# Kernel optimization log

Measured on AMD Instinct MI355X. Metric: run time of the kernel, lower is better.

Reference implementation:

```python
import jax, jax.numpy as jnp
import numpy as np
from itertools import combinations

S = 7                       # number of species (H,C,N,O,S,F,Cl)
RCR, RCA = 5.2, 3.5         # radial / angular cutoffs (Angstrom)
ETA_R, ETA_A, ZETA = 19.7, 12.5, 14.1
SHF_R = jnp.asarray(0.8 + 0.275 * np.arange(16), jnp.float32)        # 16 radial shifts
SHF_A = jnp.asarray(0.8 + 0.3375 * np.arange(8), jnp.float32)        # 8 angular radial shifts
SHF_Z = jnp.asarray((np.arange(4) + 0.5) * np.pi / 4, jnp.float32)   # 4 angle shifts
NPAIR = S * (S + 1) // 2    # 28 unordered species pairs
_t = np.zeros((S, S), np.int32); _c = 0
for _a in range(S):
    for _b in range(_a, S):
        _t[_a, _b] = _t[_b, _a] = _c; _c += 1
TRIU = jnp.asarray(_t)
AEV_DIM = S * 16 + NPAIR * 32   # 1008
M, H1, H2, H3 = 8, 256, 192, 160  # ensemble size and MLP widths


def _fc(d, rc):
    # torchani cutoff_cosine, masked for safety beyond rc
    return jnp.where(d < rc, 0.5 * jnp.cos(jnp.pi * d / rc) + 0.5, 0.0)


def compute_aev(sp, coords, atom_index12, triplet_index):
    # sp:[N] int, coords:[N,3], atom_index12:[2,P] half neighbor list,
    # triplet_index:[3,T] = (center, neighbor_j, neighbor_k)
    N = sp.shape[0]
    i, j = atom_index12[0], atom_index12[1]
    dvec = coords[j] - coords[i]
    dist = jnp.sqrt((dvec * dvec).sum(-1))
    fc = _fc(dist, RCR)
    rterm = 0.25 * jnp.exp(-ETA_R * (dist[:, None] - SHF_R) ** 2) * fc[:, None]  # [P,16]
    rad = jnp.zeros((N * S, 16), rterm.dtype)
    rad = rad.at[i * S + sp[j]].add(rterm).at[j * S + sp[i]].add(rterm)
    rad = rad.reshape(N, S * 16)

    c, a, b = triplet_index[0], triplet_index[1], triplet_index[2]
    v1 = coords[a] - coords[c]
    v2 = coords[b] - coords[c]
    d1 = jnp.sqrt((v1 * v1).sum(-1))
    d2 = jnp.sqrt((v2 * v2).sum(-1))
    cosang = 0.95 * (v1 * v2).sum(-1) / (d1 * d2)   # 0.95 numerical-safety factor as in torchani
    ang = jnp.arccos(cosang)
    fcj = _fc(d1, RCA) * _fc(d2, RCA)
    f1 = ((1.0 + jnp.cos(ang[:, None] - SHF_Z)) / 2.0) ** ZETA              # [T,4]
    f2 = jnp.exp(-ETA_A * ((d1 + d2)[:, None] / 2.0 - SHF_A) ** 2)          # [T,8]
    aterm = 2.0 * (f2[:, :, None] * f1[:, None, :]).reshape(-1, 32) * fcj[:, None]  # [T,32]
    pidx = TRIU[sp[a], sp[b]]
    angv = jnp.zeros((N * NPAIR, 32), aterm.dtype).at[c * NPAIR + pidx].add(aterm)
    return jnp.concatenate([rad, angv.reshape(N, NPAIR * 32)], axis=-1)     # [N,1008]


def _energy_and_force(species, coordinates, atom_index12, triplet_index, sgp,
                      W1, b1, W2, b2, W3, b3, W4, b4, sae):
    sp = species[0]
    sgpv = sgp[0]

    def total(coords):
        aev = compute_aev(sp, coords[0], atom_index12, triplet_index)       # [N,1008]
        h = jax.nn.celu(jnp.einsum('na,msab->msnb', aev, W1) + b1[:, :, None, :], alpha=0.1)
        h = jax.nn.celu(jnp.einsum('msnb,msbc->msnc', h, W2) + b2[:, :, None, :], alpha=0.1)
        h = jax.nn.celu(jnp.einsum('msnc,mscd->msnd', h, W3) + b3[:, :, None, :], alpha=0.1)
        e = jnp.einsum('msnd,msd->msn', h, W4) + b4[:, :, None]             # [M,S,N]
        onehot = (sgpv[None, :] == jnp.arange(S)[:, None]).astype(e.dtype)  # ghosts (-1) -> all-zero
        atomic = (e * onehot[None]).sum(1).mean(0)                           # [N] ensemble mean
        atomic = atomic + jnp.where(sgpv >= 0, sae[jnp.clip(sgpv, 0)], 0.0)  # energy shifter SAEs
        return atomic.sum()

    E = total(coordinates)
    force = -jax.grad(total)(coordinates)   # autograd force as in forward_total
    return E[None], force


def setup_inputs() -> dict:
    key = jax.random.key(0)
    n = 14; N = n ** 3   # 2744 atoms on a jittered cubic lattice (2.5 A spacing)
    ar = np.arange(n)
    gx, gy, gz = np.meshgrid(ar, ar, ar, indexing='ij')
    pos = np.stack([gx, gy, gz], -1).reshape(-1, 3)
    lid = lambda p: (p[:, 0] * n + p[:, 1]) * n + p[:, 2]
    # half neighbor list: all lattice offsets with |r| <= 5.2/2.5 lattice units
    half = [(1,0,0),(0,1,0),(0,0,1),(1,1,0),(1,-1,0),(1,0,1),(1,0,-1),(0,1,1),(0,1,-1),
            (1,1,1),(1,1,-1),(1,-1,1),(1,-1,-1),(2,0,0),(0,2,0),(0,0,2)]
    ei, ej = [], []
    for off in half:
        q = pos + np.array(off)
        m = ((q >= 0) & (q < n)).all(1)
        ei.append(lid(pos[m])); ej.append(lid(q[m]))
    atom_index12 = np.stack([np.concatenate(ei), np.concatenate(ej)]).astype(np.int32)
    # angular triplets: pairs of unit-offset neighbors (within Rca=3.5 A) per center
    unit = [(1,0,0),(-1,0,0),(0,1,0),(0,-1,0),(0,0,1),(0,0,-1)]
    nb = np.full((N, 6), -1, np.int64)
    for t, off in enumerate(unit):
        q = pos + np.array(off)
        m = ((q >= 0) & (q < n)).all(1)
        nb[lid(pos[m]), t] = lid(q[m])
    tc, tj, tk = [], [], []
    for a_, b_ in combinations(range(6), 2):
        m = (nb[:, a_] >= 0) & (nb[:, b_] >= 0)
        tc.append(np.nonzero(m)[0]); tj.append(nb[m, a_]); tk.append(nb[m, b_])
    triplet_index = np.stack([np.concatenate(tc), np.concatenate(tj), np.concatenate(tk)]).astype(np.int32)
    rng = np.random.default_rng(0)
    species = rng.integers(0, S, (1, N)).astype(np.int32)
    nghost = 250
    sgp = species.copy(); sgp[0, N - nghost:] = -1   # ghost atoms padded with -1
    coords = (pos.astype(np.float32) * 2.5 + 0.15 * rng.standard_normal((N, 3)).astype(np.float32))[None]
    ks = jax.random.split(key, 9)
    D = AEV_DIM
    W1 = jax.random.normal(ks[0], (M, S, D, H1), jnp.float32) * (D ** -0.5)
    b1 = 0.01 * jax.random.normal(ks[1], (M, S, H1), jnp.float32)
    W2 = jax.random.normal(ks[2], (M, S, H1, H2), jnp.float32) * (H1 ** -0.5)
    b2 = 0.01 * jax.random.normal(ks[3], (M, S, H2), jnp.float32)
    W3 = jax.random.normal(ks[4], (M, S, H2, H3), jnp.float32) * (H2 ** -0.5)
    b3 = 0.01 * jax.random.normal(ks[5], (M, S, H3), jnp.float32)
    W4 = jax.random.normal(ks[6], (M, S, H3), jnp.float32) * (H3 ** -0.5)
    b4 = 0.01 * jax.random.normal(ks[7], (M, S), jnp.float32)
    sae = jax.random.normal(ks[8], (S,), jnp.float32)
    return {
        'species': jnp.asarray(species), 'coordinates': jnp.asarray(coords),
        'atom_index12': jnp.asarray(atom_index12), 'triplet_index': jnp.asarray(triplet_index),
        'species_ghost_as_padding': jnp.asarray(sgp),
        'W1': W1, 'b1': b1, 'W2': W2, 'b2': b2, 'W3': W3, 'b3': b3, 'W4': W4, 'b4': b4, 'sae': sae,
    }


def reference(species, coordinates, atom_index12, triplet_index, species_ghost_as_padding,
              W1, b1, W2, b2, W3, b3, W4, b4, sae):
    return _energy_and_force(species, coordinates, atom_index12, triplet_index,
                             species_ghost_as_padding, W1, b1, W2, b2, W3, b3, W4, b4, sae)
```

## Files before the change

kernel.cpp:

```cpp
#include <hip/hip_runtime.h>
#include <math.h>

constexpr int SPEC = 7;
constexpr int DAEV = 1008;
constexpr int RADN = 112;
constexpr int H1W = 256, H2W = 192, H3W = 160;
constexpr int MENS = 8;
constexpr float ALPHA = 0.1f;
constexpr float RCR_ = 5.2f, RCA_ = 3.5f;
constexpr float ETAR = 19.7f, ETAA = 12.5f, ZETA_ = 14.1f;
constexpr float PIF = 3.14159265358979323846f;

enum { MODE_FWD = 0, MODE_BWD = 1, MODE_PLAIN = 2 };

typedef _Float16 f16x8 __attribute__((ext_vector_type(8)));
typedef float f32x4 __attribute__((ext_vector_type(4)));

__device__ __forceinline__ f32x4 mfma16(f16x8 a, f16x8 b, f32x4 c) {
    return __builtin_amdgcn_mfma_f32_16x16x32_f16(a, b, c, 0, 0, 0);
}

__device__ __forceinline__ void cvt8(float4 u0, float4 u1, f16x8& h, f16x8& l) {
    float x[8] = {u0.x, u0.y, u0.z, u0.w, u1.x, u1.y, u1.z, u1.w};
    #pragma unroll
    for (int e = 0; e < 8; ++e) {
        _Float16 hh = (_Float16)x[e];
        h[e] = hh;
        l[e] = (_Float16)(x[e] - (float)hh);
    }
}

__global__ __launch_bounds__(256) void build_lists_k(
    const int* __restrict__ sgp, int* __restrict__ counts,
    int* __restrict__ lists, int N)
{
    int n = blockIdx.x * blockDim.x + threadIdx.x;
    if (n >= N) return;
    int g = sgp[n];
    if (g >= 0) {
        int p = atomicAdd(&counts[g], 1);
        lists[g * N + p] = n;
    }
}

__global__ __launch_bounds__(256) void radial_fwd_k(
    const int* __restrict__ ai12, const int* __restrict__ spec,
    const float* __restrict__ coord, float* __restrict__ aev, int P)
{
    int p = blockIdx.x * blockDim.x + threadIdx.x;
    if (p >= P) return;
    int i = ai12[p], j = ai12[P + p];
    float dx = coord[3 * j + 0] - coord[3 * i + 0];
    float dy = coord[3 * j + 1] - coord[3 * i + 1];
    float dz = coord[3 * j + 2] - coord[3 * i + 2];
    float d = sqrtf(dx * dx + dy * dy + dz * dz);
    float fc = (d < RCR_) ? (0.5f * cosf(PIF * d / RCR_) + 0.5f) : 0.f;
    int spi = spec[i], spj = spec[j];
    float* bi = aev + (size_t)i * DAEV + spj * 16;
    float* bj = aev + (size_t)j * DAEV + spi * 16;
    #pragma unroll
    for (int k = 0; k < 16; ++k) {
        float sh = 0.8f + 0.275f * k;
        float t = d - sh;
        float v = 0.25f * expf(-ETAR * t * t) * fc;
        atomicAdd(bi + k, v);
        atomicAdd(bj + k, v);
    }
}

__global__ __launch_bounds__(256) void angular_fwd_k(
    const int* __restrict__ tri, const int* __restrict__ spec,
    const float* __restrict__ coord, float* __restrict__ aev, int T)
{
    int t = blockIdx.x * blockDim.x + threadIdx.x;
    if (t >= T) return;
    int c = tri[t], a = tri[T + t], b = tri[2 * T + t];
    float cx = coord[3 * c], cy = coord[3 * c + 1], cz = coord[3 * c + 2];
    float v1x = coord[3 * a] - cx, v1y = coord[3 * a + 1] - cy, v1z = coord[3 * a + 2] - cz;
    float v2x = coord[3 * b] - cx, v2y = coord[3 * b + 1] - cy, v2z = coord[3 * b + 2] - cz;
    float d1 = sqrtf(v1x * v1x + v1y * v1y + v1z * v1z);
    float d2 = sqrtf(v2x * v2x + v2y * v2y + v2z * v2z);
    float u = v1x * v2x + v1y * v2y + v1z * v2z;
    float ca = 0.95f * u / (d1 * d2);
    float sa = sqrtf(fmaxf(1.f - ca * ca, 0.f));
    float fc1 = (d1 < RCA_) ? (0.5f * cosf(PIF * d1 / RCA_) + 0.5f) : 0.f;
    float fc2 = (d2 < RCA_) ? (0.5f * cosf(PIF * d2 / RCA_) + 0.5f) : 0.f;
    float fcj = fc1 * fc2;
    float savg = 0.5f * (d1 + d2);
    int s1 = spec[a], s2 = spec[b];
    int lo = min(s1, s2), hi = max(s1, s2);
    int pidx = lo * SPEC - (lo * (lo - 1)) / 2 + (hi - lo);
    float* ob = aev + (size_t)c * DAEV + RADN + pidx * 32;
    const float CZ[4] = {0.92387953f, 0.38268343f, -0.38268343f, -0.92387953f};
    const float SZ[4] = {0.38268343f, 0.92387953f, 0.92387953f, 0.38268343f};
    float f1[4];
    #pragma unroll
    for (int zz = 0; zz < 4; ++zz) {
        float cd = ca * CZ[zz] + sa * SZ[zz];
        float base = fmaxf(0.5f * (1.f + cd), 0.f);
        f1[zz] = powf(base, ZETA_);
    }
    #pragma unroll
    for (int q = 0; q < 8; ++q) {
        float sh = 0.8f + 0.3375f * q;
        float tq = savg - sh;
        float f2 = expf(-ETAA * tq * tq);
        float b2 = 2.f * f2 * fcj;
        #pragma unroll
        for (int zz = 0; zz < 4; ++zz)
            atomicAdd(ob + q * 4 + zz, b2 * f1[zz]);
    }
}

template<bool DO_O, bool DO_T>
__global__ __launch_bounds__(256) void wconv_k(
    const float* __restrict__ W,
    _Float16* __restrict__ oH, _Float16* __restrict__ oL,
    _Float16* __restrict__ tH, _Float16* __restrict__ tL,
    int K, int C, int ldt)
{
    __shared__ _Float16 sh[64][65];
    __shared__ _Float16 sl[64][65];
    const int z = blockIdx.z;
    const int k0 = blockIdx.y * 64, c0 = blockIdx.x * 64;
    const float* Wz = W + (size_t)z * K * C;
    const int c = threadIdx.x & 63, qr = threadIdx.x >> 6;
    #pragma unroll
    for (int rr = 0; rr < 16; ++rr) {
        int r = qr * 16 + rr;
        int k = k0 + r, cc = c0 + c;
        float v = (k < K && cc < C) ? Wz[(size_t)k * C + cc] : 0.f;
        _Float16 h = (_Float16)v;
        _Float16 l = (_Float16)(v - (float)h);
        if (DO_O && k < K && cc < C) {
            oH[(size_t)z * K * C + (size_t)k * C + cc] = h;
            oL[(size_t)z * K * C + (size_t)k * C + cc] = l;
        }
        if (DO_T) { sh[r][c] = h; sl[r][c] = l; }
    }
    if (DO_T) {
        __syncthreads();
        #pragma unroll
        for (int rr = 0; rr < 16; ++rr) {
            int r = qr * 16 + rr;
            int crow = c0 + r, kcol = k0 + c;
            if (crow < C && kcol < ldt) {
                tH[(size_t)z * C * ldt + (size_t)crow * ldt + kcol] = sh[c][r];
                tL[(size_t)z * C * ldt + (size_t)crow * ldt + kcol] = sl[c][r];
            }
        }
    }
}

template<int MODE, int ASRC, int BSRC, bool MCONCAT, int SPLITK>
__global__ __launch_bounds__(256) void mgemm_k(
    const void* __restrict__ Ah_, const void* __restrict__ Al_,
    const void* __restrict__ Bh_, const void* __restrict__ Bl_,
    const float* __restrict__ bias, float* __restrict__ cF,
    _Float16* __restrict__ cH, _Float16* __restrict__ cL,
    const int* __restrict__ lists, const int* __restrict__ counts,
    int N, int K, int KA, int H, int lda, int ldb, int ldc,
    size_t aStrM, size_t bStrZ, size_t cStrM)
{
    __shared__ f16x8 AhS[4][64];
    __shared__ f16x8 AlS[4][64];
    __shared__ f16x8 BhS[4][128];
    __shared__ f16x8 BlS[4][128];
    __shared__ int atomsS[64];

    const int z = blockIdx.z;
    int m, sp_, chunk;
    if (MCONCAT) {
        sp_ = (SPLITK > 1) ? (z % SPEC) : z;
        chunk = (SPLITK > 1) ? (z / SPEC) : 0;
        m = 0;
    } else {
        m = z / SPEC; sp_ = z - m * SPEC; chunk = 0;
    }
    const int cnt = counts[sp_];
    const int row0 = blockIdx.y * 64;
    if (row0 >= cnt) return;
    const int col0 = blockIdx.x * 128;
    const int tid = threadIdx.x;
    const int w = tid >> 6, lane = tid & 63;

    const int rA = min(row0 + lane, cnt - 1);
    const int atomA = lists[sp_ * N + rA];
    if (tid < 64) atomsS[tid] = atomA;

    const int bc0 = min(col0 + lane, H - 1);
    const int bc1 = min(col0 + 64 + lane, H - 1);

    f16x8 rAh, rAl;
    float4 rAf0, rAf1;
    f16x8 rBh0, rBl0, rBh1, rBl1;
    float4 rBq[4];
    float rB0f[8], rB1f[8];

    auto LOAD = [&](int k0s) {
        int kk = k0s + w * 8;
        if constexpr (ASRC == 0) {
            const _Float16* ah = (const _Float16*)Ah_;
            const _Float16* al = (const _Float16*)Al_;
            size_t ao;
            if constexpr (MCONCAT) {
                int mm = kk >> 8, kr = kk & 255;
                ao = ((size_t)mm * N + atomA) * (size_t)lda + kr;
            } else {
                ao = (size_t)m * aStrM + (size_t)atomA * lda + kk;
            }
            rAh = *(const f16x8*)(ah + ao);
            rAl = *(const f16x8*)(al + ao);
        } else {
            const float* af = (const float*)Ah_;
            if (kk < KA) {
                const float* p = af + (size_t)atomA * lda + kk;
                rAf0 = *(const float4*)p;
                rAf1 = *(const float4*)(p + 4);
            } else {
                rAf0 = make_float4(0.f, 0.f, 0.f, 0.f);
                rAf1 = rAf0;
            }
        }
        if constexpr (BSRC == 0) {
            const _Float16* bh = (const _Float16*)Bh_;
            const _Float16* bl = (const _Float16*)Bl_;
            size_t b0 = (size_t)z * bStrZ + (size_t)bc0 * ldb + kk;
            size_t b1 = (size_t)z * bStrZ + (size_t)bc1 * ldb + kk;
            rBh0 = *(const f16x8*)(bh + b0);
            rBh1 = *(const f16x8*)(bh + b1);
            rBl0 = *(const f16x8*)(bl + b0);
            rBl1 = *(const f16x8*)(bl + b1);
        } else if constexpr (BSRC == 1) {
            const float* bf = (const float*)Bh_;
            int mm = kk >> 8, kr = kk & 255;
            size_t b0 = ((size_t)(mm * SPEC + sp_) * DAEV + bc0) * (size_t)ldb + kr;
            size_t b1 = ((size_t)(mm * SPEC + sp_) * DAEV + bc1) * (size_t)ldb + kr;
            rBq[0] = *(const float4*)(bf + b0);
            rBq[1] = *(const float4*)(bf + b0 + 4);
            rBq[2] = *(const float4*)(bf + b1);
            rBq[3] = *(const float4*)(bf + b1 + 4);
        } else {
            const float* bf = (const float*)Bh_ + (size_t)z * bStrZ;
            #pragma unroll
            for (int j = 0; j < 8; ++j) {
                int kg = kk + j;
                float v0 = 0.f, v1 = 0.f;
                if (kg < KA) {
                    v0 = bf[(size_t)kg * ldb + bc0];
                    v1 = bf[(size_t)kg * ldb + bc1];
                }
                rB0f[j] = v0;
                rB1f[j] = v1;
            }
        }
    };

    auto WRITE = [&]() {
        if constexpr (ASRC == 0) {
            AhS[w][lane] = rAh;
            AlS[w][lane] = rAl;
        } else {
            f16x8 h, l;
            cvt8(rAf0, rAf1, h, l);
            AhS[w][lane] = h;
            AlS[w][lane] = l;
        }
        if constexpr (BSRC == 0) {
            BhS[w][lane] = rBh0;
            BhS[w][64 + lane] = rBh1;
            BlS[w][lane] = rBl0;
            BlS[w][64 + lane] = rBl1;
        } else if constexpr (BSRC == 1) {
            f16x8 h, l;
            cvt8(rBq[0], rBq[1], h, l);
            BhS[w][lane] = h;
            BlS[w][lane] = l;
            cvt8(rBq[2], rBq[3], h, l);
            BhS[w][64 + lane] = h;
            BlS[w][64 + lane] = l;
        } else {
            f16x8 h0, l0, h1, l1;
            #pragma unroll
            for (int j = 0; j < 8; ++j) {
                _Float16 ha = (_Float16)rB0f[j];
                h0[j] = ha; l0[j] = (_Float16)(rB0f[j] - (float)ha);
                _Float16 hb = (_Float16)rB1f[j];
                h1[j] = hb; l1[j] = (_Float16)(rB1f[j] - (float)hb);
            }
            BhS[w][lane] = h0;
            BlS[w][lane] = l0;
            BhS[w][64 + lane] = h1;
            BlS[w][64 + lane] = l1;
        }
    };

    const int wr = w >> 1, wc = w & 1;
    const int fr = lane & 15, q = lane >> 4;

    f32x4 acc[2][4];
    #pragma unroll
    for (int mi = 0; mi < 2; ++mi)
        #pragma unroll
        for (int ni = 0; ni < 4; ++ni)
            acc[mi][ni] = (f32x4){0.f, 0.f, 0.f, 0.f};

    const int KC = (SPLITK > 1) ? (K / SPLITK) : K;
    const int kbeg = chunk * KC;
    const int nt = KC / 32;
    LOAD(kbeg);

    for (int t = 0; t < nt; ++t) {
        __syncthreads();
        WRITE();
        __syncthreads();
        if (t + 1 < nt) LOAD(kbeg + (t + 1) * 32);

        f16x8 fah[2], fal[2], fbh[4], fbl[4];
        #pragma unroll
        for (int mi = 0; mi < 2; ++mi) {
            int r = wr * 32 + mi * 16 + fr;
            fah[mi] = AhS[q][r];
            fal[mi] = AlS[q][r];
        }
        #pragma unroll
        for (int ni = 0; ni < 4; ++ni) {
            int c = wc * 64 + ni * 16 + fr;
            fbh[ni] = BhS[q][c];
            fbl[ni] = BlS[q][c];
        }
        #pragma unroll
        for (int mi = 0; mi < 2; ++mi)
            #pragma unroll
            for (int ni = 0; ni < 4; ++ni) {
                acc[mi][ni] = mfma16(fah[mi], fbl[ni], acc[mi][ni]);
                acc[mi][ni] = mfma16(fal[mi], fbh[ni], acc[mi][ni]);
                acc[mi][ni] = mfma16(fah[mi], fbh[ni], acc[mi][ni]);
            }
    }

    const float* brow = (MODE == MODE_FWD) ? (bias + (size_t)z * H) : nullptr;
    #pragma unroll
    for (int mi = 0; mi < 2; ++mi) {
        #pragma unroll
        for (int r = 0; r < 4; ++r) {
            int rl = wr * 32 + mi * 16 + q * 4 + r;
            if (row0 + rl >= cnt) continue;
            int atom = atomsS[rl];
            size_t rowoff = (size_t)m * cStrM + (size_t)atom * ldc;
            #pragma unroll
            for (int ni = 0; ni < 4; ++ni) {
                int col = col0 + wc * 64 + ni * 16 + fr;
                if (col >= H) continue;
                float v = acc[mi][ni][r];
                size_t idx = rowoff + col;
                if (MODE == MODE_FWD) {
                    v += brow[col];
                    v = (v > 0.f) ? v : ALPHA * expm1f(v * (1.f / ALPHA));
                    _Float16 hh = (_Float16)v;
                    cH[idx] = hh;
                    cL[idx] = (_Float16)(v - (float)hh);
                } else if (MODE == MODE_BWD) {
                    float hprev = (float)cH[idx] + (float)cL[idx];
                    float D = (hprev > 0.f) ? 1.f : (hprev * (1.f / ALPHA) + 1.f);
                    v *= D;
                    _Float16 hh = (_Float16)v;
                    cH[idx] = hh;
                    cL[idx] = (_Float16)(v - (float)hh);
                } else {
                    if (SPLITK > 1) atomicAdd(cF + idx, v);
                    else cF[idx] = v;
                }
            }
        }
    }
}

__global__ __launch_bounds__(256) void l4_k(
    _Float16* __restrict__ h3H, _Float16* __restrict__ h3L,
    const float* __restrict__ W4, const float* __restrict__ b4,
    const int* __restrict__ lists, const int* __restrict__ counts,
    float* __restrict__ Eout, int N)
{
    const int z = blockIdx.y;
    const int m = z / SPEC, s = z - m * SPEC;
    const int cnt = counts[s];
    const int sub = threadIdx.x >> 3;
    const int l8 = threadIdx.x & 7;
    const int row = blockIdx.x * 32 + sub;

    __shared__ float bsum;
    if (threadIdx.x == 0) bsum = 0.f;
    __syncthreads();

    if (row < cnt) {
        int atom = lists[s * N + row];
        size_t base = ((size_t)m * N + atom) * H3W;
        const float* w4 = W4 + (size_t)z * H3W;
        float sum = 0.f;
        for (int k = l8; k < H3W; k += 8) {
            float h = (float)h3H[base + k] + (float)h3L[base + k];
            float wv = w4[k];
            sum += h * wv;
            float D = (h > 0.f) ? 1.f : (h * 10.f + 1.f);
            float g = 0.125f * wv * D;
            _Float16 gh = (_Float16)g;
            h3H[base + k] = gh;
            h3L[base + k] = (_Float16)(g - (float)gh);
        }
        sum += __shfl_xor(sum, 1);
        sum += __shfl_xor(sum, 2);
        sum += __shfl_xor(sum, 4);
        if (l8 == 0) atomicAdd(&bsum, sum + b4[z]);
    }
    __syncthreads();
    if (threadIdx.x == 0) atomicAdd(Eout, 0.125f * bsum);
}

__global__ __launch_bounds__(256) void radial_bwd_k(
    const int* __restrict__ ai12, const int* __restrict__ spec,
    const float* __restrict__ coord, const float* __restrict__ daev,
    float* __restrict__ grad, int P)
{
    int p = blockIdx.x * blockDim.x + threadIdx.x;
    if (p >= P) return;
    int i = ai12[p], j = ai12[P + p];
    float dx = coord[3 * j + 0] - coord[3 * i + 0];
    float dy = coord[3 * j + 1] - coord[3 * i + 1];
    float dz = coord[3 * j + 2] - coord[3 * i + 2];
    float d = sqrtf(dx * dx + dy * dy + dz * dz);
    float fc, dfc;
    if (d < RCR_) {
        float ph = PIF * d / RCR_;
        fc = 0.5f * cosf(ph) + 0.5f;
        dfc = -0.5f * sinf(ph) * (PIF / RCR_);
    } else { fc = 0.f; dfc = 0.f; }
    int spi = spec[i], spj = spec[j];
    const float* gi = daev + (size_t)i * DAEV + spj * 16;
    const float* gj = daev + (size_t)j * DAEV + spi * 16;
    float gs = 0.f;
    #pragma unroll
    for (int k = 0; k < 16; ++k) {
        float sh = 0.8f + 0.275f * k;
        float t = d - sh;
        float ex = expf(-ETAR * t * t);
        float g = gi[k] + gj[k];
        gs += g * 0.25f * ex * (dfc - 2.f * ETAR * t * fc);
    }
    float invd = 1.f / d;
    float gx = gs * dx * invd, gy = gs * dy * invd, gz = gs * dz * invd;
    atomicAdd(&grad[3 * j + 0], gx);  atomicAdd(&grad[3 * j + 1], gy);  atomicAdd(&grad[3 * j + 2], gz);
    atomicAdd(&grad[3 * i + 0], -gx); atomicAdd(&grad[3 * i + 1], -gy); atomicAdd(&grad[3 * i + 2], -gz);
}

__global__ __launch_bounds__(256) void angular_bwd_k(
    const int* __restrict__ tri, const int* __restrict__ spec,
    const float* __restrict__ coord, const float* __restrict__ daev,
    float* __restrict__ grad, int T)
{
    int t = blockIdx.x * blockDim.x + threadIdx.x;
    if (t >= T) return;
    int c = tri[t], a = tri[T + t], b = tri[2 * T + t];
    float cx = coord[3 * c], cy = coord[3 * c + 1], cz = coord[3 * c + 2];
    float v1x = coord[3 * a] - cx, v1y = coord[3 * a + 1] - cy, v1z = coord[3 * a + 2] - cz;
    float v2x = coord[3 * b] - cx, v2y = coord[3 * b + 1] - cy, v2z = coord[3 * b + 2] - cz;
    float d1 = sqrtf(v1x * v1x + v1y * v1y + v1z * v1z);
    float d2 = sqrtf(v2x * v2x + v2y * v2y + v2z * v2z);
    float u = v1x * v2x + v1y * v2y + v1z * v2z;
    float inv12 = 1.f / (d1 * d2);
    float ca = 0.95f * u * inv12;
    float sa = sqrtf(fmaxf(1.f - ca * ca, 1e-12f));
    float fc1, dfc1, fc2, dfc2;
    if (d1 < RCA_) {
        float ph = PIF * d1 / RCA_;
        fc1 = 0.5f * cosf(ph) + 0.5f;
        dfc1 = -0.5f * sinf(ph) * (PIF / RCA_);
    } else { fc1 = 0.f; dfc1 = 0.f; }
    if (d2 < RCA_) {
        float ph = PIF * d2 / RCA_;
        fc2 = 0.5f * cosf(ph) + 0.5f;
        dfc2 = -0.5f * sinf(ph) * (PIF / RCA_);
    } else { fc2 = 0.f; dfc2 = 0.f; }
    float fcj = fc1 * fc2;
    float savg = 0.5f * (d1 + d2);
    int s1 = spec[a], s2 = spec[b];
    int lo = min(s1, s2), hi = max(s1, s2);
    int pidx = lo * SPEC - (lo * (lo - 1)) / 2 + (hi - lo);
    const float* gb = daev + (size_t)c * DAEV + RADN + pidx * 32;
    const float CZ[4] = {0.92387953f, 0.38268343f, -0.38268343f, -0.92387953f};
    const float SZ[4] = {0.38268343f, 0.92387953f, 0.92387953f, 0.38268343f};
    float f1[4], df1[4];
    #pragma unroll
    for (int zz = 0; zz < 4; ++zz) {
        float cd = ca * CZ[zz] + sa * SZ[zz];
        float sd = sa * CZ[zz] - ca * SZ[zz];
        float base = fmaxf(0.5f * (1.f + cd), 0.f);
        float pm1 = powf(base, ZETA_ - 1.f);
        f1[zz] = pm1 * base;
        df1[zz] = ZETA_ * pm1 * (-0.5f * sd);
    }
    float A_ = 0.f, B_ = 0.f, Cc = 0.f;
    #pragma unroll
    for (int q = 0; q < 8; ++q) {
        float sh = 0.8f + 0.3375f * q;
        float tq = savg - sh;
        float f2 = expf(-ETAA * tq * tq);
        float df2 = -ETAA * tq * f2;
        #pragma unroll
        for (int zz = 0; zz < 4; ++zz) {
            float G2 = 2.f * gb[q * 4 + zz];
            A_ += G2 * f2 * df1[zz];
            B_ += G2 * df2 * f1[zz];
            Cc += G2 * f2 * f1[zz];
        }
    }
    A_ *= fcj; B_ *= fcj;
    float C1 = Cc * dfc1 * fc2;
    float C2 = Cc * fc1 * dfc2;
    float cA = -A_ / sa;
    float k12 = cA * 0.95f * inv12;
    float coef1 = (cA * (-ca) / d1 + B_ + C1) / d1;
    float coef2 = (cA * (-ca) / d2 + B_ + C2) / d2;
    float g1x = coef1 * v1x + k12 * v2x;
    float g1y = coef1 * v1y + k12 * v2y;
    float g1z = coef1 * v1z + k12 * v2z;
    float g2x = coef2 * v2x + k12 * v1x;
    float g2y = coef2 * v2y + k12 * v1y;
    float g2z = coef2 * v2z + k12 * v1z;
    atomicAdd(&grad[3 * a + 0], g1x); atomicAdd(&grad[3 * a + 1], g1y); atomicAdd(&grad[3 * a + 2], g1z);
    atomicAdd(&grad[3 * b + 0], g2x); atomicAdd(&grad[3 * b + 1], g2y); atomicAdd(&grad[3 * b + 2], g2z);
    atomicAdd(&grad[3 * c + 0], -(g1x + g2x));
    atomicAdd(&grad[3 * c + 1], -(g1y + g2y));
    atomicAdd(&grad[3 * c + 2], -(g1z + g2z));
}

__global__ __launch_bounds__(256) void finalize_k(
    const float* __restrict__ grad, const int* __restrict__ sgp,
    const float* __restrict__ sae, float* __restrict__ out, int N)
{
    int n = blockIdx.x * blockDim.x + threadIdx.x;
    __shared__ float bs;
    if (threadIdx.x == 0) bs = 0.f;
    __syncthreads();
    float v = 0.f;
    if (n < N) {
        out[1 + 3 * n + 0] = -grad[3 * n + 0];
        out[1 + 3 * n + 1] = -grad[3 * n + 1];
        out[1 + 3 * n + 2] = -grad[3 * n + 2];
        int g = sgp[n];
        if (g >= 0) v = sae[g];
    }
    atomicAdd(&bs, v);
    __syncthreads();
    if (threadIdx.x == 0) atomicAdd(out, bs);
}

extern "C" void kernel_launch(void* const* d_in, const int* in_sizes, int n_in,
                              void* d_out, int out_size, void* d_ws, size_t ws_size,
                              hipStream_t stream)
{
    (void)n_in; (void)out_size; (void)ws_size;
    const int* species = (const int*)d_in[0];
    const float* coords = (const float*)d_in[1];
    const int* ai12 = (const int*)d_in[2];
    const int* tri = (const int*)d_in[3];
    const int* sgp = (const int*)d_in[4];
    const float* W1 = (const float*)d_in[5];
    const float* b1 = (const float*)d_in[6];
    const float* W2 = (const float*)d_in[7];
    const float* b2 = (const float*)d_in[8];
    const float* W3 = (const float*)d_in[9];
    const float* b3 = (const float*)d_in[10];
    const float* W4 = (const float*)d_in[11];
    const float* b4 = (const float*)d_in[12];
    const float* sae = (const float*)d_in[13];
    float* out = (float*)d_out;

    const int N = in_sizes[0];
    const int P = in_sizes[2] / 2;
    const int T = in_sizes[3] / 3;
    const size_t NM = (size_t)MENS * N;

    float* ws = (float*)d_ws;
    size_t off = 0;
    auto alloc = [&](size_t nf) { float* p = ws + off; off += nf; return p; };

    float* aev = alloc((size_t)N * DAEV);
    _Float16* H1h = (_Float16*)alloc(NM * 128);
    _Float16* H1l = (_Float16*)alloc(NM * 128);
    _Float16* H2h = (_Float16*)alloc(NM * 96);
    _Float16* H2l = (_Float16*)alloc(NM * 96);
    _Float16* H3h = (_Float16*)alloc(NM * 80);
    _Float16* H3l = (_Float16*)alloc(NM * 80);
    _Float16* Wh = (_Float16*)alloc((size_t)56 * 96 * 256);
    _Float16* Wl = (_Float16*)alloc((size_t)56 * 96 * 256);
    float* grad = alloc((size_t)N * 3);
    int* counts = (int*)alloc(8);
    int* lists = (int*)alloc((size_t)SPEC * N);
    float* daev = aev;

    hipMemsetAsync(aev, 0, (size_t)N * DAEV * sizeof(float), stream);
    hipMemsetAsync(grad, 0, (size_t)N * 3 * sizeof(float), stream);
    hipMemsetAsync(counts, 0, 8 * sizeof(int), stream);
    hipMemsetAsync(d_out, 0, sizeof(float), stream);

    build_lists_k<<<(N + 255) / 256, 256, 0, stream>>>(sgp, counts, lists, N);
    radial_fwd_k<<<(P + 255) / 256, 256, 0, stream>>>(ai12, species, coords, aev, P);
    angular_fwd_k<<<(T + 255) / 256, 256, 0, stream>>>(tri, species, coords, aev, T);

    const int rt = (N + 63) / 64;

    mgemm_k<MODE_FWD, 1, 2, false, 1><<<dim3(2, rt, 56), 256, 0, stream>>>(
        aev, nullptr, W1, nullptr, b1, nullptr, H1h, H1l,
        lists, counts, N, 1024, 1008, 256, 1008, 256, 256,
        0, (size_t)1008 * 256, (size_t)N * 256);

    wconv_k<false, true><<<dim3(3, 4, 56), 256, 0, stream>>>(
        W2, nullptr, nullptr, Wh, Wl, 256, 192, 256);
    mgemm_k<MODE_FWD, 0, 0, false, 1><<<dim3(2, rt, 56), 256, 0, stream>>>(
        H1h, H1l, Wh, Wl, b2, nullptr, H2h, H2l,
        lists, counts, N, 256, 256, 192, 256, 256, 192,
        (size_t)N * 256, (size_t)192 * 256, (size_t)N * 192);

    wconv_k<false, true><<<dim3(3, 3, 56), 256, 0, stream>>>(
        W3, nullptr, nullptr, Wh, Wl, 192, 160, 192);
    mgemm_k<MODE_FWD, 0, 0, false, 1><<<dim3(2, rt, 56), 256, 0, stream>>>(
        H2h, H2l, Wh, Wl, b3, nullptr, H3h, H3l,
        lists, counts, N, 192, 192, 160, 192, 192, 160,
        (size_t)N * 192, (size_t)160 * 192, (size_t)N * 160);

    l4_k<<<dim3((N + 31) / 32, 56), 256, 0, stream>>>(
        H3h, H3l, W4, b4, lists, counts, out, N);

    hipMemsetAsync(daev, 0, (size_t)N * DAEV * sizeof(float), stream);

    wconv_k<true, false><<<dim3(3, 3, 56), 256, 0, stream>>>(
        W3, Wh, Wl, nullptr, nullptr, 192, 160, 0);
    mgemm_k<MODE_BWD, 0, 0, false, 1><<<dim3(2, rt, 56), 256, 0, stream>>>(
        H3h, H3l, Wh, Wl, nullptr, nullptr, H2h, H2l,
        lists, counts, N, 160, 160, 192, 160, 160, 192,
        (size_t)N * 160, (size_t)192 * 160, (size_t)N * 192);

    wconv_k<true, false><<<dim3(3, 4, 56), 256, 0, stream>>>(
        W2, Wh, Wl, nullptr, nullptr, 256, 192, 0);
    mgemm_k<MODE_BWD, 0, 0, false, 1><<<dim3(2, rt, 56), 256, 0, stream>>>(
        H2h, H2l, Wh, Wl, nullptr, nullptr, H1h, H1l,
        lists, counts, N, 192, 192, 256, 192, 192, 256,
        (size_t)N * 192, (size_t)256 * 192, (size_t)N * 256);

    mgemm_k<MODE_PLAIN, 0, 1, true, 4><<<dim3(8, rt, 28), 256, 0, stream>>>(
        H1h, H1l, W1, nullptr, nullptr, daev, nullptr, nullptr,
        lists, counts, N, 2048, 2048, 1008, 256, 256, 1008,
        0, 0, 0);

    radial_bwd_k<<<(P + 255) / 256, 256, 0, stream>>>(ai12, species, coords, daev, grad, P);
    angular_bwd_k<<<(T + 255) / 256, 256, 0, stream>>>(tri, species, coords, daev, grad, T);
    finalize_k<<<(N + 255) / 256, 256, 0, stream>>>(grad, sgp, sae, out, N);
}
```

Measured before the change: 779.1 us.

## Split GEMM K-loop across two wave groups and remap blocks per XCD

The per-species MLP GEMM kernel now runs 512 threads, with two groups of four waves each handling half of the K tiles in separate shared-memory buffers. The partial accumulators are then reduced through shared memory before the epilogue. This doubles the waves per output tile to hide load latency and shortens each tile's serial K loop. For grids with 56 z-slices, block indices are also remapped so blocks sharing a z (same weight matrix) land on the same XCD, aiming for better L2 reuse. The cost is extra LDS traffic for the reduction, more barriers, and higher register pressure under the 512-thread launch bound.

```diff
diff --git a/kernel.cpp b/kernel.cpp
--- a/kernel.cpp
+++ b/kernel.cpp
@@ -153,7 +153,7 @@
 }
 
 template<int MODE, int ASRC, int BSRC, bool MCONCAT, int SPLITK>
-__global__ __launch_bounds__(256) void mgemm_k(
+__global__ __launch_bounds__(512) void mgemm_k(
     const void* __restrict__ Ah_, const void* __restrict__ Al_,
     const void* __restrict__ Bh_, const void* __restrict__ Bl_,
     const float* __restrict__ bias, float* __restrict__ cF,
@@ -162,13 +162,27 @@
     int N, int K, int KA, int H, int lda, int ldb, int ldc,
     size_t aStrM, size_t bStrZ, size_t cStrM)
 {
-    __shared__ f16x8 AhS[4][64];
-    __shared__ f16x8 AlS[4][64];
-    __shared__ f16x8 BhS[4][128];
-    __shared__ f16x8 BlS[4][128];
+    __shared__ f16x8 SM[3072];
     __shared__ int atomsS[64];
-
-    const int z = blockIdx.z;
+    #define AhS(g, kq, i) SM[(g) * 256 + (kq) * 64 + (i)]
+    #define AlS(g, kq, i) SM[512 + (g) * 256 + (kq) * 64 + (i)]
+    #define BhS(g, kq, c) SM[1024 + (g) * 512 + (kq) * 128 + (c)]
+    #define BlS(g, kq, c) SM[2048 + (g) * 512 + (kq) * 128 + (c)]
+
+    int bx = blockIdx.x, by = blockIdx.y, bz = blockIdx.z;
+    if (gridDim.z == 56) {
+        int BXY = gridDim.x * gridDim.y;
+        int flat = bx + gridDim.x * (by + gridDim.y * bz);
+        int xcd = flat & 7;
+        int rest = flat >> 3;
+        int zw = rest / BXY;
+        int xy = rest - zw * BXY;
+        bz = xcd * 7 + zw;
+        bx = xy % gridDim.x;
+        by = xy / gridDim.x;
+    }
+
+    const int z = bz;
     int m, sp_, chunk;
     if (MCONCAT) {
         sp_ = (SPLITK > 1) ? (z % SPEC) : z;
@@ -178,11 +192,12 @@
         m = z / SPEC; sp_ = z - m * SPEC; chunk = 0;
     }
     const int cnt = counts[sp_];
-    const int row0 = blockIdx.y * 64;
+    const int row0 = by * 64;
     if (row0 >= cnt) return;
-    const int col0 = blockIdx.x * 128;
+    const int col0 = bx * 128;
     const int tid = threadIdx.x;
     const int w = tid >> 6, lane = tid & 63;
+    const int g = w >> 2, wl = w & 3;
 
     const int rA = min(row0 + lane, cnt - 1);
     const int atomA = lists[sp_ * N + rA];
@@ -198,7 +213,7 @@
     float rB0f[8], rB1f[8];
 
     auto LOAD = [&](int k0s) {
-        int kk = k0s + w * 8;
+        int kk = k0s + wl * 8;
         if constexpr (ASRC == 0) {
             const _Float16* ah = (const _Float16*)Ah_;
             const _Float16* al = (const _Float16*)Al_;
@@ -258,27 +273,27 @@
 
     auto WRITE = [&]() {
         if constexpr (ASRC == 0) {
-            AhS[w][lane] = rAh;
-            AlS[w][lane] = rAl;
+            AhS(g, wl, lane) = rAh;
+            AlS(g, wl, lane) = rAl;
         } else {
             f16x8 h, l;
             cvt8(rAf0, rAf1, h, l);
-            AhS[w][lane] = h;
-            AlS[w][lane] = l;
+            AhS(g, wl, lane) = h;
+            AlS(g, wl, lane) = l;
         }
         if constexpr (BSRC == 0) {
-            BhS[w][lane] = rBh0;
-            BhS[w][64 + lane] = rBh1;
-            BlS[w][lane] = rBl0;
-            BlS[w][64 + lane] = rBl1;
+            BhS(g, wl, lane) = rBh0;
+            BhS(g, wl, 64 + lane) = rBh1;
+            BlS(g, wl, lane) = rBl0;
+            BlS(g, wl, 64 + lane) = rBl1;
         } else if constexpr (BSRC == 1) {
             f16x8 h, l;
             cvt8(rBq[0], rBq[1], h, l);
-            BhS[w][lane] = h;
-            BlS[w][lane] = l;
+            BhS(g, wl, lane) = h;
+            BlS(g, wl, lane) = l;
             cvt8(rBq[2], rBq[3], h, l);
-            BhS[w][64 + lane] = h;
-            BlS[w][64 + lane] = l;
+            BhS(g, wl, 64 + lane) = h;
+            BlS(g, wl, 64 + lane) = l;
         } else {
             f16x8 h0, l0, h1, l1;
             #pragma unroll
@@ -288,14 +303,14 @@
                 _Float16 hb = (_Float16)rB1f[j];
                 h1[j] = hb; l1[j] = (_Float16)(rB1f[j] - (float)hb);
             }
-            BhS[w][lane] = h0;
-            BlS[w][lane] = l0;
-            BhS[w][64 + lane] = h1;
-            BlS[w][64 + lane] = l1;
+            BhS(g, wl, lane) = h0;
+            BlS(g, wl, lane) = l0;
+            BhS(g, wl, 64 + lane) = h1;
+            BlS(g, wl, 64 + lane) = l1;
         }
     };
 
-    const int wr = w >> 1, wc = w & 1;
+    const int wr = wl >> 1, wc = wl & 1;
     const int fr = lane & 15, q = lane >> 4;
 
     f32x4 acc[2][4];
@@ -307,37 +322,63 @@
 
     const int KC = (SPLITK > 1) ? (K / SPLITK) : K;
     const int kbeg = chunk * KC;
-    const int nt = KC / 32;
-    LOAD(kbeg);
-
-    for (int t = 0; t < nt; ++t) {
+    const int ntT = KC / 32;
+    const int nt0 = (ntT + 1) >> 1;
+    const int my_nt = g ? (ntT - nt0) : nt0;
+    const int gk = kbeg + (g ? nt0 * 32 : 0);
+
+    if (my_nt > 0) LOAD(gk);
+
+    for (int t = 0; t < nt0; ++t) {
         __syncthreads();
-        WRITE();
+        if (t < my_nt) WRITE();
         __syncthreads();
-        if (t + 1 < nt) LOAD(kbeg + (t + 1) * 32);
-
-        f16x8 fah[2], fal[2], fbh[4], fbl[4];
-        #pragma unroll
-        for (int mi = 0; mi < 2; ++mi) {
-            int r = wr * 32 + mi * 16 + fr;
-            fah[mi] = AhS[q][r];
-            fal[mi] = AlS[q][r];
-        }
-        #pragma unroll
-        for (int ni = 0; ni < 4; ++ni) {
-            int c = wc * 64 + ni * 16 + fr;
-            fbh[ni] = BhS[q][c];
-            fbl[ni] = BlS[q][c];
-        }
+        if (t + 1 < my_nt) LOAD(gk + (t + 1) * 32);
+
+        if (t < my_nt) {
+            f16x8 fah[2], fal[2], fbh[4], fbl[4];
+            #pragma unroll
+            for (int mi = 0; mi < 2; ++mi) {
+                int r = wr * 32 + mi * 16 + fr;
+                fah[mi] = AhS(g, q, r);
+                fal[mi] = AlS(g, q, r);
+            }
+            #pragma unroll
+            for (int ni = 0; ni < 4; ++ni) {
+                int c = wc * 64 + ni * 16 + fr;
+                fbh[ni] = BhS(g, q, c);
+                fbl[ni] = BlS(g, q, c);
+            }
+            #pragma unroll
+            for (int mi = 0; mi < 2; ++mi)
+                #pragma unroll
+                for (int ni = 0; ni < 4; ++ni) {
+                    acc[mi][ni] = mfma16(fah[mi], fbl[ni], acc[mi][ni]);
+                    acc[mi][ni] = mfma16(fal[mi], fbh[ni], acc[mi][ni]);
+                    acc[mi][ni] = mfma16(fah[mi], fbh[ni], acc[mi][ni]);
+                }
+        }
+    }
+
+    __syncthreads();
+    f32x4* X = (f32x4*)SM;
+    const int xbase = (wl * 64 + lane) * 8;
+    if (g == 1) {
         #pragma unroll
         for (int mi = 0; mi < 2; ++mi)
             #pragma unroll
-            for (int ni = 0; ni < 4; ++ni) {
-                acc[mi][ni] = mfma16(fah[mi], fbl[ni], acc[mi][ni]);
-                acc[mi][ni] = mfma16(fal[mi], fbh[ni], acc[mi][ni]);
-                acc[mi][ni] = mfma16(fah[mi], fbh[ni], acc[mi][ni]);
-            }
-    }
+            for (int ni = 0; ni < 4; ++ni)
+                X[xbase + mi * 4 + ni] = acc[mi][ni];
+    }
+    __syncthreads();
+    if (g == 1) return;
+    #pragma unroll
+    for (int mi = 0; mi < 2; ++mi)
+        #pragma unroll
+        for (int ni = 0; ni < 4; ++ni) {
+            f32x4 o = X[xbase + mi * 4 + ni];
+            acc[mi][ni] += o;
+        }
 
     const float* brow = (MODE == MODE_FWD) ? (bias + (size_t)z * H) : nullptr;
     #pragma unroll
@@ -374,6 +415,10 @@
             }
         }
     }
+    #undef AhS
+    #undef AlS
+    #undef BhS
+    #undef BlS
 }
 
 __global__ __launch_bounds__(256) void l4_k(
@@ -610,21 +655,21 @@
 
     const int rt = (N + 63) / 64;
 
-    mgemm_k<MODE_FWD, 1, 2, false, 1><<<dim3(2, rt, 56), 256, 0, stream>>>(
+    mgemm_k<MODE_FWD, 1, 2, false, 1><<<dim3(2, rt, 56), 512, 0, stream>>>(
         aev, nullptr, W1, nullptr, b1, nullptr, H1h, H1l,
         lists, counts, N, 1024, 1008, 256, 1008, 256, 256,
         0, (size_t)1008 * 256, (size_t)N * 256);
 
     wconv_k<false, true><<<dim3(3, 4, 56), 256, 0, stream>>>(
         W2, nullptr, nullptr, Wh, Wl, 256, 192, 256);
-    mgemm_k<MODE_FWD, 0, 0, false, 1><<<dim3(2, rt, 56), 256, 0, stream>>>(
+    mgemm_k<MODE_FWD, 0, 0, false, 1><<<dim3(2, rt, 56), 512, 0, stream>>>(
         H1h, H1l, Wh, Wl, b2, nullptr, H2h, H2l,
         lists, counts, N, 256, 256, 192, 256, 256, 192,
         (size_t)N * 256, (size_t)192 * 256, (size_t)N * 192);
 
     wconv_k<false, true><<<dim3(3, 3, 56), 256, 0, stream>>>(
         W3, nullptr, nullptr, Wh, Wl, 192, 160, 192);
-    mgemm_k<MODE_FWD, 0, 0, false, 1><<<dim3(2, rt, 56), 256, 0, stream>>>(
+    mgemm_k<MODE_FWD, 0, 0, false, 1><<<dim3(2, rt, 56), 512, 0, stream>>>(
         H2h, H2l, Wh, Wl, b3, nullptr, H3h, H3l,
         lists, counts, N, 192, 192, 160, 192, 192, 160,
         (size_t)N * 192, (size_t)160 * 192, (size_t)N * 160);
@@ -636,19 +681,19 @@
 
     wconv_k<true, false><<<dim3(3, 3, 56), 256, 0, stream>>>(
         W3, Wh, Wl, nullptr, nullptr, 192, 160, 0);
-    mgemm_k<MODE_BWD, 0, 0, false, 1><<<dim3(2, rt, 56), 256, 0, stream>>>(
+    mgemm_k<MODE_BWD, 0, 0, false, 1><<<dim3(2, rt, 56), 512, 0, stream>>>(
         H3h, H3l, Wh, Wl, nullptr, nullptr, H2h, H2l,
         lists, counts, N, 160, 160, 192, 160, 160, 192,
         (size_t)N * 160, (size_t)192 * 160, (size_t)N * 192);
 
     wconv_k<true, false><<<dim3(3, 4, 56), 256, 0, stream>>>(
         W2, Wh, Wl, nullptr, nullptr, 256, 192, 0);
-    mgemm_k<MODE_BWD, 0, 0, false, 1><<<dim3(2, rt, 56), 256, 0, stream>>>(
+    mgemm_k<MODE_BWD, 0, 0, false, 1><<<dim3(2, rt, 56), 512, 0, stream>>>(
         H2h, H2l, Wh, Wl, nullptr, nullptr, H1h, H1l,
         lists, counts, N, 192, 192, 256, 192, 192, 256,
         (size_t)N * 192, (size_t)256 * 192, (size_t)N * 256);
 
-    mgemm_k<MODE_PLAIN, 0, 1, true, 4><<<dim3(8, rt, 28), 256, 0, stream>>>(
+    mgemm_k<MODE_PLAIN, 0, 1, true, 4><<<dim3(8, rt, 28), 512, 0, stream>>>(
         H1h, H1l, W1, nullptr, nullptr, daev, nullptr, nullptr,
         lists, counts, N, 2048, 2048, 1008, 256, 256, 1008,
         0, 0, 0);
```

After: 795.9 us. +2.1%, slower.
